# Kernel tuning notes

Hardware: AMD Instinct MI355X
Metric: run time of the kernel (lower is better)

Reference implementation:

```python
import jax, jax.numpy as jnp
import numpy as np

K = 20  # kNN fan-out


def knn_idx(x, k):
    # x: (B, C, N). Negative squared pairwise distance; top-k largest = nearest.
    inner = -2.0 * jnp.einsum('bcn,bcm->bnm', x, x)        # (B, N, N)
    xx = jnp.sum(x * x, axis=1)                            # (B, N)
    pd = -xx[:, :, None] - inner - xx[:, None, :]          # (B, N, N)
    return jax.lax.top_k(pd, k)[1]                         # (B, N, k) int32


def get_graph_feature(x, k):
    # x: (B, C, N) -> edge features (B, 2C, N, k)
    idx = knn_idx(x, k)                                    # (B, N, k)
    xt = jnp.transpose(x, (0, 2, 1))                       # (B, N, C)
    nbrs = jax.vmap(lambda pts, ids: pts[ids])(xt, idx)    # (B, N, k, C)
    center = xt[:, :, None, :]                             # (B, N, 1, C)
    feat = jnp.concatenate(
        [nbrs - center, jnp.broadcast_to(center, nbrs.shape)], axis=-1)  # (B,N,k,2C)
    return jnp.transpose(feat, (0, 3, 1, 2))               # (B, 2C, N, k)


def vn_layer(W, x):
    # W: (out, in); x: (B, in, N, k) -> (B, out, N, k)
    return jnp.einsum('oi,bink->bonk', W, x)


def setup_inputs() -> dict:
    key = jax.random.key(0)
    ks = jax.random.split(key, 6)
    B, C, N = 16, 3, 2048
    num_classes = 10
    return {
        'x': jax.random.normal(ks[0], (B, C, N), dtype=jnp.float32),
        'W1': jax.random.normal(ks[1], (64, 6), dtype=jnp.float32),
        'W2': jax.random.normal(ks[2], (128, 64), dtype=jnp.float32),
        'W3': jax.random.normal(ks[3], (256, 128), dtype=jnp.float32),
        'fc_w': jax.random.normal(ks[4], (num_classes, 256), dtype=jnp.float32) * 0.0625,
        'fc_b': jax.random.normal(ks[5], (num_classes,), dtype=jnp.float32) * 0.0625,
    }


def reference(x, W1, W2, W3, fc_w, fc_b):
    h = get_graph_feature(x, K)          # (B, 6, N, k)
    h = vn_layer(W1, h)                  # (B, 64, N, k)
    h = jax.nn.relu(vn_layer(W2, h))     # (B, 128, N, k)
    h = jax.nn.relu(vn_layer(W3, h))     # (B, 256, N, k)
    h = jnp.max(h, axis=-1)              # max over neighbors k -> (B, 256, N)
    h = jnp.max(h, axis=-1)              # global max over points -> (B, 256)
    return h @ fc_w.T + fc_b             # (B, num_classes)
```

## Files before the change

### kernel.cpp

```cpp
#include <hip/hip_runtime.h>
#include <stdint.h>

typedef short v8s __attribute__((ext_vector_type(8)));
typedef float v4f __attribute__((ext_vector_type(4)));

#define NPTS 2048
#define BATCH 16
#define KNN 20
#define PAIRS (NPTS * KNN)

__device__ __forceinline__ unsigned bf16pack2(float lo, float hi) {
  unsigned ul = __float_as_uint(lo), uh = __float_as_uint(hi);
  return ((ul + 0x8000u) >> 16) | ((uh + 0x8000u) & 0xffff0000u);
}
__device__ __forceinline__ unsigned pair_h2(unsigned pu, unsigned qu) {
  float pl = __uint_as_float(pu << 16);
  float ph = __uint_as_float(pu & 0xffff0000u);
  float ql = __uint_as_float(qu << 16);
  float qh = __uint_as_float(qu & 0xffff0000u);
  return bf16pack2(fmaxf(pl + ql, 0.f), fmaxf(ph + qh, 0.f));
}

__global__ void prep_kernel(const float* __restrict__ W1, const float* __restrict__ W2,
                            float* __restrict__ M2a, float* __restrict__ M2b,
                            int* __restrict__ H) {
  if (blockIdx.x == 0 && threadIdx.x < 128) {
    int o = threadIdx.x;
    float a0 = 0, a1 = 0, a2 = 0, b0 = 0, b1 = 0, b2 = 0;
    for (int i = 0; i < 64; ++i) {
      float w2 = W2[o * 64 + i];
      const float* w1r = W1 + i * 6;
      a0 += w2 * w1r[0]; a1 += w2 * w1r[1]; a2 += w2 * w1r[2];
      b0 += w2 * (w1r[3] - w1r[0]); b1 += w2 * (w1r[4] - w1r[1]); b2 += w2 * (w1r[5] - w1r[2]);
    }
    M2a[o * 3 + 0] = a0; M2a[o * 3 + 1] = a1; M2a[o * 3 + 2] = a2;
    M2b[o * 3 + 0] = b0; M2b[o * 3 + 1] = b1; M2b[o * 3 + 2] = b2;
  }
  int g = blockIdx.x * 128 + threadIdx.x;
  if (g < BATCH * 256) H[g] = 0;
}

__global__ __launch_bounds__(64) void pq_kernel(const float* __restrict__ x,
                                                const float* __restrict__ M2a,
                                                const float* __restrict__ M2b,
                                                unsigned short* __restrict__ p,
                                                unsigned short* __restrict__ q) {
  int b = blockIdx.x >> 6;
  int j0 = (blockIdx.x & 63) << 5;
  int t = threadIdx.x;
  int o0 = t * 2;
  float a00 = M2a[o0 * 3 + 0], a01 = M2a[o0 * 3 + 1], a02 = M2a[o0 * 3 + 2];
  float a10 = M2a[o0 * 3 + 3], a11 = M2a[o0 * 3 + 4], a12 = M2a[o0 * 3 + 5];
  float b00 = M2b[o0 * 3 + 0], b01 = M2b[o0 * 3 + 1], b02 = M2b[o0 * 3 + 2];
  float b10 = M2b[o0 * 3 + 3], b11 = M2b[o0 * 3 + 4], b12 = M2b[o0 * 3 + 5];
  const float* xb = x + b * 3 * NPTS;
  unsigned* pw = (unsigned*)p;
  unsigned* qw = (unsigned*)q;
  for (int jj = 0; jj < 32; ++jj) {
    int j = j0 + jj;
    float x0 = xb[j], x1 = xb[NPTS + j], x2 = xb[2 * NPTS + j];
    float p0 = a00 * x0 + a01 * x1 + a02 * x2;
    float p1 = a10 * x0 + a11 * x1 + a12 * x2;
    float q0 = b00 * x0 + b01 * x1 + b02 * x2;
    float q1 = b10 * x0 + b11 * x1 + b12 * x2;
    size_t base = ((size_t)(b * NPTS + j)) * 64 + t;
    pw[base] = bf16pack2(p0, p1);
    qw[base] = bf16pack2(q0, q1);
  }
}

__global__ __launch_bounds__(256) void knn_kernel(const float* __restrict__ x,
                                                  int* __restrict__ idxOut) {
  __shared__ float px[NPTS], py[NPTS], pz[NPTS];
  __shared__ unsigned long long cand[4][128];
  int b = blockIdx.x >> 9;
  int qb = (blockIdx.x & 511) << 2;
  const float* xb = x + b * 3 * NPTS;
  for (int i = threadIdx.x; i < NPTS; i += 256) {
    px[i] = xb[i]; py[i] = xb[NPTS + i]; pz[i] = xb[2 * NPTS + i];
  }
  __syncthreads();
  int wid = threadIdx.x >> 6, lane = threadIdx.x & 63;
  int qn = qb + wid;
  float qx = px[qn], qy = py[qn], qz = pz[qn];

  float mymin = 1e30f;
#pragma unroll
  for (int s = 0; s < 32; ++s) {
    int i = s * 64 + lane;
    float dx = px[i] - qx, dy = py[i] - qy, dz = pz[i] - qz;
    float d = dx * dx + dy * dy + dz * dz;
    mymin = fminf(mymin, d);
  }
  float v = mymin;
  for (int k = 2; k <= 64; k <<= 1) {
    for (int j = k >> 1; j > 0; j >>= 1) {
      float o = __shfl_xor(v, j);
      bool low = (lane & j) == 0;
      bool up = (lane & k) == 0;
      v = (low == up) ? fminf(v, o) : fmaxf(v, o);
    }
  }
  float tau = __shfl(v, 19);
  tau = tau * (1.0f + 3.8e-6f);

  int base = 0;
#pragma unroll
  for (int s = 0; s < 32; ++s) {
    int i = s * 64 + lane;
    float dx = px[i] - qx, dy = py[i] - qy, dz = pz[i] - qz;
    float d = dx * dx + dy * dy + dz * dz;
    bool take = d <= tau;
    unsigned long long mb = __ballot(take);
    if (take) {
      int pos = base + __popcll(mb & ((1ull << lane) - 1ull));
      if (pos < 128)
        cand[wid][pos] = (((unsigned long long)__float_as_uint(d)) << 32) | (unsigned)i;
    }
    base += __popcll(mb);
  }
  int nc = base < 128 ? base : 128;
  __syncthreads();

  unsigned long long k0 = (lane < nc) ? cand[wid][lane] : ~0ull;
  unsigned long long k1 = (lane + 64 < nc) ? cand[wid][lane + 64] : ~0ull;
  int r0 = 0, r1 = 0;
  for (int i = 0; i < nc; ++i) {
    unsigned long long ki = cand[wid][i];
    r0 += (ki < k0) ? 1 : 0;
    r1 += (ki < k1) ? 1 : 0;
  }
  long long obase = ((long long)b * NPTS + qn) * KNN;
  if (lane < nc && r0 < KNN) idxOut[obase + r0] = (int)(k0 & 0xffffffffu);
  if (lane + 64 < nc && r1 < KNN) idxOut[obase + r1] = (int)(k1 & 0xffffffffu);
}

__global__ __launch_bounds__(256, 2) void gemm_max_kernel(
    const unsigned short* __restrict__ p, const unsigned short* __restrict__ q,
    const int* __restrict__ idx, const float* __restrict__ W3, int* __restrict__ H) {
  __shared__ __align__(16) unsigned short h2s[2][16 * 136];

  int b = blockIdx.x & 15;
  int w = blockIdx.x >> 4;
  int t = threadIdx.x;
  int lane = t & 63, wid = t >> 6;
  int r16 = lane & 15, quad = lane >> 4;

  v8s bfr[4][4];
#pragma unroll
  for (int ntl = 0; ntl < 4; ++ntl) {
#pragma unroll
    for (int kk = 0; kk < 4; ++kk) {
      int n = (wid * 4 + ntl) * 16 + r16;
      const float* src = W3 + n * 128 + kk * 32 + quad * 8;
      v8s f;
#pragma unroll
      for (int jj = 0; jj < 8; ++jj)
        f[jj] = (short)((__float_as_uint(src[jj]) + 0x8000u) >> 16);
      bfr[ntl][kk] = f;
    }
  }

  const unsigned short* pB = p + (size_t)b * NPTS * 128;
  const unsigned short* qB = q + (size_t)b * NPTS * 128;
  const int* idxB = idx + (size_t)b * PAIRS;

  int pm = t >> 4;
  int cseg = t & 15;

  uint4 P4n, Q4n;
  {
    int pr = w * 16 + pm;
    int n0 = pr / 20;
    int j0 = idxB[pr] & (NPTS - 1);
    P4n = *(const uint4*)(pB + (size_t)j0 * 128 + cseg * 8);
    Q4n = *(const uint4*)(qB + (size_t)n0 * 128 + cseg * 8);
  }

  float vmx[4] = {0.f, 0.f, 0.f, 0.f};
  int buf = 0;
  for (int T = w; T < PAIRS / 16; T += 48) {
    uint4 R;
    R.x = pair_h2(P4n.x, Q4n.x);
    R.y = pair_h2(P4n.y, Q4n.y);
    R.z = pair_h2(P4n.z, Q4n.z);
    R.w = pair_h2(P4n.w, Q4n.w);
    *(uint4*)&h2s[buf][pm * 136 + cseg * 8] = R;
    __syncthreads();

    int Tn = T + 48;
    if (Tn < PAIRS / 16) {
      int prn = Tn * 16 + pm;
      int nn = prn / 20;
      int jn = idxB[prn] & (NPTS - 1);
      P4n = *(const uint4*)(pB + (size_t)jn * 128 + cseg * 8);
      Q4n = *(const uint4*)(qB + (size_t)nn * 128 + cseg * 8);
    }

    v8s a[4];
#pragma unroll
    for (int kk = 0; kk < 4; ++kk)
      a[kk] = *(const v8s*)&h2s[buf][r16 * 136 + kk * 32 + quad * 8];

#pragma unroll
    for (int ntl = 0; ntl < 4; ++ntl) {
      v4f acc = {0.f, 0.f, 0.f, 0.f};
#pragma unroll
      for (int kk = 0; kk < 4; ++kk)
        acc = __builtin_amdgcn_mfma_f32_16x16x32_bf16(a[kk], bfr[ntl][kk], acc, 0, 0, 0);
      vmx[ntl] = fmaxf(vmx[ntl], fmaxf(fmaxf(acc[0], acc[1]), fmaxf(acc[2], acc[3])));
    }
    buf ^= 1;
  }

#pragma unroll
  for (int ntl = 0; ntl < 4; ++ntl) {
    float vv = vmx[ntl];
    vv = fmaxf(vv, __shfl_xor(vv, 16));
    vv = fmaxf(vv, __shfl_xor(vv, 32));
    if (quad == 0) {
      int ch = (wid * 4 + ntl) * 16 + r16;
      atomicMax(&H[b * 256 + ch], __float_as_int(vv));
    }
  }
}

__global__ void fc_kernel(const int* __restrict__ Hi, const float* __restrict__ fcw,
                          const float* __restrict__ fcb, float* __restrict__ out) {
  int t = threadIdx.x;
  if (t >= BATCH * 10) return;
  int b = t / 10, r = t % 10;
  const float* Hb = (const float*)Hi + b * 256;
  float s = fcb[r];
  for (int c = 0; c < 256; ++c) s += Hb[c] * fcw[r * 256 + c];
  out[b * 10 + r] = s;
}

extern "C" void kernel_launch(void* const* d_in, const int* in_sizes, int n_in,
                              void* d_out, int out_size, void* d_ws, size_t ws_size,
                              hipStream_t stream) {
  const float* x   = (const float*)d_in[0];
  const float* W1  = (const float*)d_in[1];
  const float* W2  = (const float*)d_in[2];
  const float* W3  = (const float*)d_in[3];
  const float* fcw = (const float*)d_in[4];
  const float* fcb = (const float*)d_in[5];
  float* out = (float*)d_out;
  char* ws = (char*)d_ws;

  float* M2a = (float*)(ws + 0);
  float* M2b = (float*)(ws + 1536);
  int* H     = (int*)(ws + 4096);
  int* idx   = (int*)(ws + 24576);
  unsigned short* p = (unsigned short*)(ws + 3145728);
  unsigned short* q = (unsigned short*)(ws + 12582912);

  prep_kernel<<<32, 128, 0, stream>>>(W1, W2, M2a, M2b, H);
  pq_kernel<<<BATCH * 64, 64, 0, stream>>>(x, M2a, M2b, p, q);
  knn_kernel<<<BATCH * 512, 256, 0, stream>>>(x, idx);
  gemm_max_kernel<<<BATCH * 48, 256, 0, stream>>>(p, q, idx, W3, H);
  fc_kernel<<<1, 256, 0, stream>>>(H, fcw, fcb, out);
}
```

Measured before the change: 197.2 us.

## Batch four queries per wave in kNN, double gemm grid, parallelize FC

Each wave in the kNN kernel now handles four query points, so every shared-memory point load is reused across four distance computations. This also cuts the grid 4x, so the per-block staging of all 2048 points into LDS happens far less often. The gemm_max kernel launches twice as many blocks with a stride of 96 to raise occupancy and parallelism. The FC kernel moves from one block of scalar loops to one wave per output with a shuffle reduction. The cost is more registers and a larger candidate buffer in the kNN kernel, plus fewer kNN blocks in flight.

```diff
diff --git a/kernel.cpp b/kernel.cpp
--- a/kernel.cpp
+++ b/kernel.cpp
@@ -72,67 +72,84 @@
 __global__ __launch_bounds__(256) void knn_kernel(const float* __restrict__ x,
                                                   int* __restrict__ idxOut) {
   __shared__ float px[NPTS], py[NPTS], pz[NPTS];
-  __shared__ unsigned long long cand[4][128];
-  int b = blockIdx.x >> 9;
-  int qb = (blockIdx.x & 511) << 2;
+  __shared__ unsigned long long cand[4][4][128];
+  int b = blockIdx.x >> 7;
+  int qblk = blockIdx.x & 127;
   const float* xb = x + b * 3 * NPTS;
   for (int i = threadIdx.x; i < NPTS; i += 256) {
     px[i] = xb[i]; py[i] = xb[NPTS + i]; pz[i] = xb[2 * NPTS + i];
   }
   __syncthreads();
   int wid = threadIdx.x >> 6, lane = threadIdx.x & 63;
-  int qn = qb + wid;
-  float qx = px[qn], qy = py[qn], qz = pz[qn];
-
-  float mymin = 1e30f;
-#pragma unroll
+  int qbase = qblk * 16 + wid * 4;
+
+  float qx[4], qy[4], qz[4], mn[4];
+#pragma unroll
+  for (int g = 0; g < 4; ++g) {
+    qx[g] = px[qbase + g]; qy[g] = py[qbase + g]; qz[g] = pz[qbase + g];
+    mn[g] = 1e30f;
+  }
+
   for (int s = 0; s < 32; ++s) {
     int i = s * 64 + lane;
-    float dx = px[i] - qx, dy = py[i] - qy, dz = pz[i] - qz;
-    float d = dx * dx + dy * dy + dz * dz;
-    mymin = fminf(mymin, d);
-  }
-  float v = mymin;
-  for (int k = 2; k <= 64; k <<= 1) {
-    for (int j = k >> 1; j > 0; j >>= 1) {
-      float o = __shfl_xor(v, j);
-      bool low = (lane & j) == 0;
-      bool up = (lane & k) == 0;
-      v = (low == up) ? fminf(v, o) : fmaxf(v, o);
-    }
-  }
-  float tau = __shfl(v, 19);
-  tau = tau * (1.0f + 3.8e-6f);
-
-  int base = 0;
-#pragma unroll
+    float X = px[i], Y = py[i], Z = pz[i];
+#pragma unroll
+    for (int g = 0; g < 4; ++g) {
+      float dx = X - qx[g], dy = Y - qy[g], dz = Z - qz[g];
+      mn[g] = fminf(mn[g], dx * dx + dy * dy + dz * dz);
+    }
+  }
+
+  float tau[4];
+#pragma unroll
+  for (int g = 0; g < 4; ++g) {
+    float v = mn[g];
+    for (int k = 2; k <= 64; k <<= 1) {
+      for (int j = k >> 1; j > 0; j >>= 1) {
+        float o = __shfl_xor(v, j);
+        bool low = (lane & j) == 0;
+        bool up = (lane & k) == 0;
+        v = (low == up) ? fminf(v, o) : fmaxf(v, o);
+      }
+    }
+    tau[g] = __shfl(v, 19) * (1.0f + 3.8e-6f);
+  }
+
+  int cnt[4] = {0, 0, 0, 0};
   for (int s = 0; s < 32; ++s) {
     int i = s * 64 + lane;
-    float dx = px[i] - qx, dy = py[i] - qy, dz = pz[i] - qz;
-    float d = dx * dx + dy * dy + dz * dz;
-    bool take = d <= tau;
-    unsigned long long mb = __ballot(take);
-    if (take) {
-      int pos = base + __popcll(mb & ((1ull << lane) - 1ull));
-      if (pos < 128)
-        cand[wid][pos] = (((unsigned long long)__float_as_uint(d)) << 32) | (unsigned)i;
-    }
-    base += __popcll(mb);
-  }
-  int nc = base < 128 ? base : 128;
-  __syncthreads();
-
-  unsigned long long k0 = (lane < nc) ? cand[wid][lane] : ~0ull;
-  unsigned long long k1 = (lane + 64 < nc) ? cand[wid][lane + 64] : ~0ull;
-  int r0 = 0, r1 = 0;
-  for (int i = 0; i < nc; ++i) {
-    unsigned long long ki = cand[wid][i];
-    r0 += (ki < k0) ? 1 : 0;
-    r1 += (ki < k1) ? 1 : 0;
-  }
-  long long obase = ((long long)b * NPTS + qn) * KNN;
-  if (lane < nc && r0 < KNN) idxOut[obase + r0] = (int)(k0 & 0xffffffffu);
-  if (lane + 64 < nc && r1 < KNN) idxOut[obase + r1] = (int)(k1 & 0xffffffffu);
+    float X = px[i], Y = py[i], Z = pz[i];
+#pragma unroll
+    for (int g = 0; g < 4; ++g) {
+      float dx = X - qx[g], dy = Y - qy[g], dz = Z - qz[g];
+      float d = dx * dx + dy * dy + dz * dz;
+      bool take = d <= tau[g];
+      unsigned long long mb = __ballot(take);
+      if (take) {
+        int pos = cnt[g] + __popcll(mb & ((1ull << lane) - 1ull));
+        if (pos < 128)
+          cand[wid][g][pos] =
+              (((unsigned long long)__float_as_uint(d)) << 32) | (unsigned)i;
+      }
+      cnt[g] += __popcll(mb);
+    }
+  }
+
+#pragma unroll
+  for (int g = 0; g < 4; ++g) {
+    int nc = cnt[g] < 128 ? cnt[g] : 128;
+    unsigned long long k0 = (lane < nc) ? cand[wid][g][lane] : ~0ull;
+    unsigned long long k1 = (lane + 64 < nc) ? cand[wid][g][lane + 64] : ~0ull;
+    int r0 = 0, r1 = 0;
+    for (int i = 0; i < nc; ++i) {
+      unsigned long long ki = cand[wid][g][i];
+      r0 += (ki < k0) ? 1 : 0;
+      r1 += (ki < k1) ? 1 : 0;
+    }
+    long long obase = ((long long)b * NPTS + qbase + g) * KNN;
+    if (lane < nc && r0 < KNN) idxOut[obase + r0] = (int)(k0 & 0xffffffffu);
+    if (lane + 64 < nc && r1 < KNN) idxOut[obase + r1] = (int)(k1 & 0xffffffffu);
+  }
 }
 
 __global__ __launch_bounds__(256, 2) void gemm_max_kernel(
@@ -179,7 +196,7 @@
 
   float vmx[4] = {0.f, 0.f, 0.f, 0.f};
   int buf = 0;
-  for (int T = w; T < PAIRS / 16; T += 48) {
+  for (int T = w; T < PAIRS / 16; T += 96) {
     uint4 R;
     R.x = pair_h2(P4n.x, Q4n.x);
     R.y = pair_h2(P4n.y, Q4n.y);
@@ -188,7 +205,7 @@
     *(uint4*)&h2s[buf][pm * 136 + cseg * 8] = R;
     __syncthreads();
 
-    int Tn = T + 48;
+    int Tn = T + 96;
     if (Tn < PAIRS / 16) {
       int prn = Tn * 16 + pm;
       int nn = prn / 20;
@@ -225,15 +242,19 @@
   }
 }
 
-__global__ void fc_kernel(const int* __restrict__ Hi, const float* __restrict__ fcw,
-                          const float* __restrict__ fcb, float* __restrict__ out) {
-  int t = threadIdx.x;
-  if (t >= BATCH * 10) return;
-  int b = t / 10, r = t % 10;
+__global__ __launch_bounds__(64) void fc_kernel(const int* __restrict__ Hi,
+                                                const float* __restrict__ fcw,
+                                                const float* __restrict__ fcb,
+                                                float* __restrict__ out) {
+  int b = blockIdx.x / 10, r = blockIdx.x % 10;
+  int lane = threadIdx.x;
   const float* Hb = (const float*)Hi + b * 256;
-  float s = fcb[r];
-  for (int c = 0; c < 256; ++c) s += Hb[c] * fcw[r * 256 + c];
-  out[b * 10 + r] = s;
+  float s = 0.f;
+#pragma unroll
+  for (int c = lane; c < 256; c += 64) s += Hb[c] * fcw[r * 256 + c];
+#pragma unroll
+  for (int m = 32; m > 0; m >>= 1) s += __shfl_xor(s, m);
+  if (lane == 0) out[b * 10 + r] = s + fcb[r];
 }
 
 extern "C" void kernel_launch(void* const* d_in, const int* in_sizes, int n_in,
@@ -257,7 +278,7 @@
 
   prep_kernel<<<32, 128, 0, stream>>>(W1, W2, M2a, M2b, H);
   pq_kernel<<<BATCH * 64, 64, 0, stream>>>(x, M2a, M2b, p, q);
-  knn_kernel<<<BATCH * 512, 256, 0, stream>>>(x, idx);
-  gemm_max_kernel<<<BATCH * 48, 256, 0, stream>>>(p, q, idx, W3, H);
-  fc_kernel<<<1, 256, 0, stream>>>(H, fcw, fcb, out);
-}
+  knn_kernel<<<BATCH * 128, 256, 0, stream>>>(x, idx);
+  gemm_max_kernel<<<BATCH * 96, 256, 0, stream>>>(p, q, idx, W3, H);
+  fc_kernel<<<BATCH * 10, 64, 0, stream>>>(H, fcw, fcb, out);
+}
```

After: 192.8 us. -2.2%, faster.
